# Kernel tuning notes

Hardware: AMD Instinct MI355X
Metric: run time of the kernel (lower is better)

The kernel has to match this reference:

```python
import jax, jax.numpy as jnp
import numpy as np

NH, DH = 16, 64          # n_head, d_head
CH = NH + DH             # 80
RQ, RK, RV = 6, 2, 2
ROPE_BASE = 10000.0


def _rotary(b, cache_len):
    # b: [B, T, R, DH]; rotates the d-factor exactly as the torch Rotary module
    T = b.shape[1]
    inv_freq = (1.0 / ROPE_BASE) ** (jnp.arange(0, DH, 2, dtype=jnp.float32) / DH)
    t = jnp.arange(T, dtype=jnp.float32) + cache_len
    freqs = jnp.outer(t, inv_freq)                      # [T, DH/2]
    cos = freqs[None, :, None, :].astype(b.dtype)
    sin = jnp.sin(freqs)[None, :, None, :].astype(b.dtype)
    cos = jnp.cos(freqs)[None, :, None, :].astype(b.dtype)
    x1, x2 = jnp.split(b, 2, axis=3)
    return jnp.concatenate([x1 * cos + x2 * sin, -x1 * sin + x2 * cos], axis=3)


def setup_inputs() -> dict:
    key = jax.random.key(0)
    k1, k2, k3, k4 = jax.random.split(key, 4)
    B, T, D = 2, 2048, 1024
    x = jax.random.normal(k1, (B, T, D), dtype=jnp.float32)
    # xavier-uniform-like scale for factor projections
    s_q = float(np.sqrt(6.0 / (D + CH)))
    s_o = float(np.sqrt(6.0 / (D + D)))
    W_abq = jax.random.uniform(k2, (RQ * CH, D), minval=-s_q, maxval=s_q, dtype=jnp.float32)
    W_abkv = jax.random.uniform(k3, ((RK + RV) * CH, D), minval=-s_q, maxval=s_q, dtype=jnp.float32)
    W_o = jax.random.uniform(k4, (D, D), minval=-s_o, maxval=s_o, dtype=jnp.float32)
    return {"x": x, "W_abq": W_abq, "W_abkv": W_abkv, "W_o": W_o}


def reference(x, W_abq, W_abkv, W_o):
    B, T, D = x.shape
    # low-rank factor projections
    abq = (x @ W_abq.T).reshape(B, T, RQ, CH)
    a_q, b_q = abq[..., :NH], abq[..., NH:]            # [B,T,RQ,NH], [B,T,RQ,DH]
    abkv = (x @ W_abkv.T).reshape(B, T, RK + RV, CH)
    a_kv = abkv[..., :NH]
    b_kv = _rotary(abkv[..., NH:], cache_len=0)        # RoPE applied to K/V d-factors only
    a_k, b_k = a_kv[:, :, :RK], b_kv[:, :, :RK]
    a_v, b_v = a_kv[:, :, RK:], b_kv[:, :, RK:]
    # tensor-product reconstruction of Q/K/V
    q = jnp.einsum('btrh,btrd->bthd', a_q, b_q) / RQ
    k = jnp.einsum('btrh,btrd->bthd', a_k, b_k) / RK
    v = jnp.einsum('btrh,btrd->bthd', a_v, b_v) / RV
    # causal attention (flex_attention default scale = 1/sqrt(dh))
    scale = 1.0 / jnp.sqrt(jnp.asarray(DH, dtype=q.dtype))
    scores = jnp.einsum('bqhd,bkhd->bhqk', q, k) * scale
    causal = jnp.tril(jnp.ones((T, T), dtype=bool))
    scores = jnp.where(causal[None, None], scores, jnp.finfo(scores.dtype).min)
    attn = jax.nn.softmax(scores, axis=-1)
    y = jnp.einsum('bhqk,bkhd->bqhd', attn, v).reshape(B, T, D)
    return y @ W_o.T
```

## Files before the change

kernel.cpp:

```cpp
#include <hip/hip_runtime.h>
#include <hip/hip_bf16.h>
#include <math.h>

#define NHEADS 16
#define DHEAD  64
#define CHDIM  80
#define RQn    6
#define RKn    2
#define RVn    2
#define BB     2
#define TT     2048
#define DDim   1024
#define NQK    800

using frag16 = __attribute__((ext_vector_type(8))) short;
using f32x4  = __attribute__((ext_vector_type(4))) float;
using f32x16 = __attribute__((ext_vector_type(16))) float;
using uint2v = __attribute__((ext_vector_type(2))) unsigned int;

#define AS1(p) ((const __attribute__((address_space(1))) unsigned int*)(p))
#define AS3(p) ((__attribute__((address_space(3))) unsigned int*)(p))

static __device__ __forceinline__ unsigned short bf16_bits(float f) {
    __hip_bfloat16 h = __float2bfloat16(f);
    return *(unsigned short*)&h;
}
static __device__ __forceinline__ unsigned int pk2(float a, float b) {
    return ((unsigned int)bf16_bits(b) << 16) | (unsigned int)bf16_bits(a);
}
static __device__ __forceinline__ float bfu2f(unsigned short u) {
    return __uint_as_float(((unsigned int)u) << 16);
}
static __device__ __forceinline__ float exp2_hw(float x) {
    return __builtin_amdgcn_exp2f(x);
}

__global__ __launch_bounds__(256) void cvt_all(
    const float* __restrict__ x, const float* __restrict__ wq,
    const float* __restrict__ wk, const float* __restrict__ wo,
    __hip_bfloat16* __restrict__ xb, __hip_bfloat16* __restrict__ wqk,
    __hip_bfloat16* __restrict__ wob)
{
    int bid = blockIdx.x;
    const float* src; __hip_bfloat16* dst; int n4;
    if (bid < 4096)      { src = x;  dst = xb;            n4 = 1048576; }
    else if (bid < 4576) { bid -= 4096; src = wq; dst = wqk;           n4 = 122880; }
    else if (bid < 4896) { bid -= 4576; src = wk; dst = wqk + 491520;  n4 = 81920; }
    else                 { bid -= 4896; src = wo; dst = wob;           n4 = 262144; }
    int i = bid * 256 + threadIdx.x;
    if (i < n4) {
        float4 v = *(const float4*)&src[i * 4];
        ushort4 o;
        o.x = bf16_bits(v.x); o.y = bf16_bits(v.y);
        o.z = bf16_bits(v.z); o.w = bf16_bits(v.w);
        *(ushort4*)&dst[i * 4] = o;
    }
}

template <bool BF16OUT>
__global__ __launch_bounds__(256) void gemm_bf16(
    const __hip_bfloat16* __restrict__ A, const __hip_bfloat16* __restrict__ W,
    void* __restrict__ Cv, int M, int N, int K)
{
    __shared__ __hip_bfloat16 Asl[2][64 * 64];
    __shared__ __hip_bfloat16 Bsl[2][128 * 64];
    const int tid = threadIdx.x;
    const int w = tid >> 6, lane = tid & 63;
    const int l16 = lane & 15, quad = lane >> 4;
    const int bm = blockIdx.y * 64, bn = blockIdx.x * 128;

    int rSA[2], cSA[2];
    #pragma unroll
    for (int j = 0; j < 2; j++) {
        int L = (w * 2 + j) * 64 + lane;
        rSA[j] = L >> 3;
        cSA[j] = (L & 7) ^ (rSA[j] & 7);
    }
    int rSB[4], cSB[4];
    #pragma unroll
    for (int j = 0; j < 4; j++) {
        int L = (w * 4 + j) * 64 + lane;
        int r = L >> 3;
        cSB[j] = (L & 7) ^ (r & 7);
        int rb = bn + r;
        rSB[j] = (rb < N) ? rb : (N - 1);
    }

    f32x4 acc[4][2];
    #pragma unroll
    for (int mt = 0; mt < 4; mt++)
        #pragma unroll
        for (int nt = 0; nt < 2; nt++)
            acc[mt][nt] = (f32x4){0.f, 0.f, 0.f, 0.f};

    const int nK = K >> 6;
    #pragma unroll
    for (int j = 0; j < 2; j++)
        __builtin_amdgcn_global_load_lds(AS1(A + (size_t)(bm + rSA[j]) * K + cSA[j] * 8),
                                         AS3(&Asl[0][(w * 2 + j) * 512]), 16, 0, 0);
    #pragma unroll
    for (int j = 0; j < 4; j++)
        __builtin_amdgcn_global_load_lds(AS1(W + (size_t)rSB[j] * K + cSB[j] * 8),
                                         AS3(&Bsl[0][(w * 4 + j) * 512]), 16, 0, 0);

    for (int kk = 0; kk < nK; kk++) {
        const int cur = kk & 1;
        __syncthreads();
        if (kk + 1 < nK) {
            const int k1 = (kk + 1) * 64;
            #pragma unroll
            for (int j = 0; j < 2; j++)
                __builtin_amdgcn_global_load_lds(AS1(A + (size_t)(bm + rSA[j]) * K + k1 + cSA[j] * 8),
                                                 AS3(&Asl[cur ^ 1][(w * 2 + j) * 512]), 16, 0, 0);
            #pragma unroll
            for (int j = 0; j < 4; j++)
                __builtin_amdgcn_global_load_lds(AS1(W + (size_t)rSB[j] * K + k1 + cSB[j] * 8),
                                                 AS3(&Bsl[cur ^ 1][(w * 4 + j) * 512]), 16, 0, 0);
        }
        #pragma unroll
        for (int ks = 0; ks < 2; ks++) {
            frag16 af[4], bf[2];
            #pragma unroll
            for (int mt = 0; mt < 4; mt++) {
                int r = mt * 16 + l16;
                af[mt] = *(const frag16*)&Asl[cur][r * 64 + (((ks * 4 + quad) ^ (r & 7)) * 8)];
            }
            #pragma unroll
            for (int nt = 0; nt < 2; nt++) {
                int r = w * 32 + nt * 16 + l16;
                bf[nt] = *(const frag16*)&Bsl[cur][r * 64 + (((ks * 4 + quad) ^ (r & 7)) * 8)];
            }
            #pragma unroll
            for (int mt = 0; mt < 4; mt++)
                #pragma unroll
                for (int nt = 0; nt < 2; nt++)
                    acc[mt][nt] = __builtin_amdgcn_mfma_f32_16x16x32_bf16(af[mt], bf[nt], acc[mt][nt], 0, 0, 0);
        }
    }
    #pragma unroll
    for (int mt = 0; mt < 4; mt++) {
        #pragma unroll
        for (int reg = 0; reg < 4; reg++) {
            int row = bm + mt * 16 + quad * 4 + reg;
            #pragma unroll
            for (int nt = 0; nt < 2; nt++) {
                int col = bn + w * 32 + nt * 16 + l16;
                if (col < N) {
                    if constexpr (BF16OUT)
                        ((__hip_bfloat16*)Cv)[(size_t)row * N + col] = __float2bfloat16(acc[mt][nt][reg]);
                    else
                        ((float*)Cv)[(size_t)row * N + col] = acc[mt][nt][reg];
                }
            }
        }
    }
}

__global__ __launch_bounds__(256) void qkv_kernel(
    const __hip_bfloat16* __restrict__ ab,
    __hip_bfloat16* __restrict__ q, __hip_bfloat16* __restrict__ k,
    __hip_bfloat16* __restrict__ vT)
{
    const int tok0 = blockIdx.x * 4;
    const int w = threadIdx.x >> 6;
    const int d = threadIdx.x & 63;
    const int token = tok0 + w;
    const int b = token / TT;
    const int t = token % TT;
    __shared__ float sab[4][NQK];
    __shared__ __align__(8) __hip_bfloat16 vbuf[NHEADS][DHEAD][4];
    const __hip_bfloat16* aq = ab + (size_t)token * NQK;
    #pragma unroll
    for (int i2 = d; i2 < NQK / 2; i2 += 64) {
        unsigned int u = *(const unsigned int*)&aq[i2 * 2];
        sab[w][i2 * 2 + 0] = bfu2f((unsigned short)(u & 0xffff));
        sab[w][i2 * 2 + 1] = bfu2f((unsigned short)(u >> 16));
    }
    const float* sq  = sab[w];
    const float* skv = sab[w] + 480;
    const int i32 = d & 31;
    float inv_freq = exp2_hw(-(float)i32 * (13.287712379549449f / 32.0f));
    float fr = (float)t * inv_freq;
    float c = cosf(fr), s = sinf(fr);
    __syncthreads();
    float rot[4];
    #pragma unroll
    for (int r = 0; r < 4; r++) {
        float x1 = skv[r * CHDIM + NHEADS + i32];
        float x2 = skv[r * CHDIM + NHEADS + 32 + i32];
        rot[r] = (d < 32) ? (x1 * c + x2 * s) : (-x1 * s + x2 * c);
    }
    float bqv[RQn];
    #pragma unroll
    for (int r = 0; r < RQn; r++) bqv[r] = sq[r * CHDIM + NHEADS + d];
    #pragma unroll
    for (int h = 0; h < NHEADS; h++) {
        float accq = 0.0f;
        #pragma unroll
        for (int r = 0; r < RQn; r++)
            accq += sq[r * CHDIM + h] * bqv[r];
        q[((size_t)(b * NHEADS + h) * TT + t) * DHEAD + d] =
            __float2bfloat16(accq * (0.125f / 6.0f) * 1.4426950408889634f);
        float acck = 0.0f, accv = 0.0f;
        #pragma unroll
        for (int r = 0; r < RKn; r++)
            acck += skv[r * CHDIM + h] * rot[r];
        #pragma unroll
        for (int r = 0; r < RVn; r++)
            accv += skv[(RKn + r) * CHDIM + h] * rot[RKn + r];
        k[((size_t)(b * NHEADS + h) * TT + t) * DHEAD + d] = __float2bfloat16(acck * 0.5f);
        vbuf[h][d][w] = __float2bfloat16(accv * 0.5f);
    }
    __syncthreads();
    const int t0 = tok0 % TT;
    const int b0 = tok0 / TT;
    for (int row = threadIdx.x; row < NHEADS * DHEAD; row += 256) {
        int h = row >> 6, dd = row & 63;
        *(uint2*)&vT[((size_t)(b0 * NHEADS + h) * DHEAD + dd) * TT + t0] =
            *(const uint2*)&vbuf[h][dd][0];
    }
}

static __device__ __forceinline__ void build_pfrag(
    const float* s0, const float* s1, frag16 Pf[4])
{
    #pragma unroll
    for (int k2 = 0; k2 < 4; k2++) {
        const float* sF = (k2 >= 2) ? s1 : s0;
        const int bs = 8 * (k2 & 1);
        unsigned int a0 = pk2(sF[bs + 0], sF[bs + 1]);
        unsigned int b0 = pk2(sF[bs + 2], sF[bs + 3]);
        unsigned int a1 = pk2(sF[bs + 4], sF[bs + 5]);
        unsigned int b1 = pk2(sF[bs + 6], sF[bs + 7]);
        uint2v ra = __builtin_amdgcn_permlane32_swap(a0, a1, false, false);
        uint2v rb = __builtin_amdgcn_permlane32_swap(b0, b1, false, false);
        union { frag16 f; unsigned int u[4]; } pf;
        pf.u[0] = ra[0]; pf.u[1] = rb[0]; pf.u[2] = ra[1]; pf.u[3] = rb[1];
        Pf[k2] = pf.f;
    }
}

static __device__ __forceinline__ void attn_tile(
    const __hip_bfloat16* __restrict__ Kc, const __hip_bfloat16* __restrict__ Vc,
    const frag16 qB[4], f32x16& O0, f32x16& O1, float& lpart,
    const int l31, const int hi, const int xi,
    const bool domask, const int kb0, const int qlane)
{
    f32x16 ST0 = {}, ST1 = {};
    __builtin_amdgcn_s_setprio(1);
    #pragma unroll
    for (int kt4 = 0; kt4 < 4; kt4++) {
        int c8 = kt4 * 2 + hi;
        frag16 kf0 = *(const frag16*)&Kc[l31 * 64 + ((c8 ^ xi) * 8)];
        frag16 kf1 = *(const frag16*)&Kc[(32 + l31) * 64 + ((c8 ^ xi) * 8)];
        ST0 = __builtin_amdgcn_mfma_f32_32x32x16_bf16(kf0, qB[kt4], ST0, 0, 0, 0);
        ST1 = __builtin_amdgcn_mfma_f32_32x32x16_bf16(kf1, qB[kt4], ST1, 0, 0, 0);
    }
    __builtin_amdgcn_s_setprio(0);
    float* s0 = (float*)&ST0;
    float* s1 = (float*)&ST1;
    if (domask) {
        int kbq = kb0 + 4 * hi;
        #pragma unroll
        for (int reg = 0; reg < 16; reg++) {
            int rowc = (reg & 3) + 8 * (reg >> 2);
            if (kbq + rowc > qlane)      s0[reg] = -1e30f;
            if (kbq + 32 + rowc > qlane) s1[reg] = -1e30f;
        }
    }
    #pragma unroll
    for (int reg = 0; reg < 16; reg++) {
        float p0 = exp2_hw(s0[reg]);
        float p1 = exp2_hw(s1[reg]);
        s0[reg] = p0; s1[reg] = p1;
        lpart += p0 + p1;
    }
    frag16 Pf[4];
    build_pfrag(s0, s1, Pf);
    __builtin_amdgcn_s_setprio(1);
    #pragma unroll
    for (int k2 = 0; k2 < 4; k2++) {
        int c8 = k2 * 2 + hi;
        frag16 vf0 = *(const frag16*)&Vc[l31 * 64 + ((c8 ^ xi) * 8)];
        frag16 vf1 = *(const frag16*)&Vc[(32 + l31) * 64 + ((c8 ^ xi) * 8)];
        O0 = __builtin_amdgcn_mfma_f32_32x32x16_bf16(vf0, Pf[k2], O0, 0, 0, 0);
        O1 = __builtin_amdgcn_mfma_f32_32x32x16_bf16(vf1, Pf[k2], O1, 0, 0, 0);
    }
    __builtin_amdgcn_s_setprio(0);
}

static __device__ __forceinline__ void attn_tile2(
    const __hip_bfloat16* __restrict__ Kc, const __hip_bfloat16* __restrict__ Vc,
    const frag16 qBlo[4], const frag16 qBhi[4],
    f32x16& Olo0, f32x16& Olo1, float& l_lo,
    f32x16& Ohi0, f32x16& Ohi1, float& l_hi,
    const int l31, const int hi, const int xi,
    const bool domask_lo, const int kb0, const int qlane_lo)
{
    f32x16 SL0 = {}, SL1 = {}, SH0 = {}, SH1 = {};
    __builtin_amdgcn_s_setprio(1);
    #pragma unroll
    for (int kt4 = 0; kt4 < 4; kt4++) {
        int c8 = kt4 * 2 + hi;
        frag16 kf0 = *(const frag16*)&Kc[l31 * 64 + ((c8 ^ xi) * 8)];
        frag16 kf1 = *(const frag16*)&Kc[(32 + l31) * 64 + ((c8 ^ xi) * 8)];
        SL0 = __builtin_amdgcn_mfma_f32_32x32x16_bf16(kf0, qBlo[kt4], SL0, 0, 0, 0);
        SH0 = __builtin_amdgcn_mfma_f32_32x32x16_bf16(kf0, qBhi[kt4], SH0, 0, 0, 0);
        SL1 = __builtin_amdgcn_mfma_f32_32x32x16_bf16(kf1, qBlo[kt4], SL1, 0, 0, 0);
        SH1 = __builtin_amdgcn_mfma_f32_32x32x16_bf16(kf1, qBhi[kt4], SH1, 0, 0, 0);
    }
    __builtin_amdgcn_s_setprio(0);
    float* sl0 = (float*)&SL0; float* sl1 = (float*)&SL1;
    float* sh0 = (float*)&SH0; float* sh1 = (float*)&SH1;
    if (domask_lo) {
        int kbq = kb0 + 4 * hi;
        #pragma unroll
        for (int reg = 0; reg < 16; reg++) {
            int rowc = (reg & 3) + 8 * (reg >> 2);
            if (kbq + rowc > qlane_lo)      sl0[reg] = -1e30f;
            if (kbq + 32 + rowc > qlane_lo) sl1[reg] = -1e30f;
        }
    }
    #pragma unroll
    for (int reg = 0; reg < 16; reg++) {
        float a = exp2_hw(sl0[reg]); float b = exp2_hw(sl1[reg]);
        float c = exp2_hw(sh0[reg]); float d = exp2_hw(sh1[reg]);
        sl0[reg] = a; sl1[reg] = b; sh0[reg] = c; sh1[reg] = d;
        l_lo += a + b; l_hi += c + d;
    }
    frag16 PfL[4], PfH[4];
    build_pfrag(sl0, sl1, PfL);
    build_pfrag(sh0, sh1, PfH);
    __builtin_amdgcn_s_setprio(1);
    #pragma unroll
    for (int k2 = 0; k2 < 4; k2++) {
        int c8 = k2 * 2 + hi;
        frag16 vf0 = *(const frag16*)&Vc[l31 * 64 + ((c8 ^ xi) * 8)];
        frag16 vf1 = *(const frag16*)&Vc[(32 + l31) * 64 + ((c8 ^ xi) * 8)];
        Olo0 = __builtin_amdgcn_mfma_f32_32x32x16_bf16(vf0, PfL[k2], Olo0, 0, 0, 0);
        Ohi0 = __builtin_amdgcn_mfma_f32_32x32x16_bf16(vf0, PfH[k2], Ohi0, 0, 0, 0);
        Olo1 = __builtin_amdgcn_mfma_f32_32x32x16_bf16(vf1, PfL[k2], Olo1, 0, 0, 0);
        Ohi1 = __builtin_amdgcn_mfma_f32_32x32x16_bf16(vf1, PfH[k2], Ohi1, 0, 0, 0);
    }
    __builtin_amdgcn_s_setprio(0);
}

__global__ __launch_bounds__(256, 2) void flash_mfma(
    const __hip_bfloat16* __restrict__ q, const __hip_bfloat16* __restrict__ k,
    const __hip_bfloat16* __restrict__ vT, __hip_bfloat16* __restrict__ y,
    float* __restrict__ Op, float* __restrict__ Lp)
{
    const int Bid = blockIdx.x;
    const int xcd = Bid & 7;
    const int slot0 = Bid >> 3;
    const int bh = xcd * 4 + (slot0 & 3);
    const int idx0 = slot0 >> 2;
    const int qthalf = idx0 & 7;
    const int part = idx0 >> 3;
    const int qt_lo = qthalf, qt_hi = 15 - qthalf;
    const int nlo = 2 * qt_lo + 2;
    const int S = 17 - nlo;
    const int b = bh >> 4, h = bh & 15;
    const int tid = threadIdx.x;
    const int w = tid >> 6;
    const int lane = tid & 63;
    const int l31 = lane & 31;
    const int hi = lane >> 5;
    const int xi = l31 & 7;
    const int paddr = (lane ^ 32) << 2;

    __shared__ __align__(16) __hip_bfloat16 KsF[2][4096];
    __shared__ __align__(16) __hip_bfloat16 VsF[2][4096];

    const size_t base = (size_t)bh * TT * DHEAD;
    const __hip_bfloat16* qb = q + base;
    const __hip_bfloat16* kb = k + base;
    const __hip_bfloat16* vb = vT + base;

    const int ktd_lo = 2 * qt_lo + (w >> 1);
    const int ktd_hi = 2 * qt_hi + (w >> 1);
    const int qlane_lo = qt_lo * 128 + w * 32 + l31;
    const int qlane_hi = qt_hi * 128 + w * 32 + l31;

    const int k0off  = part ? S : 0;
    const int nsteps = part ? 17 : ((nlo > S) ? nlo : S);

    int offK[2], offV[2];
    #pragma unroll
    for (int j = 0; j < 2; j++) {
        int Lc = w * 128 + j * 64 + lane;
        int r = Lc >> 3, c8 = Lc & 7, g8 = c8 ^ (r & 7);
        offK[j] = r * 64 + g8 * 8;
        offV[j] = r * TT + g8 * 8;
    }

    frag16 qB_hi[4], qB_lo[4];
    #pragma unroll
    for (int kt4 = 0; kt4 < 4; kt4++)
        qB_hi[kt4] = *(const frag16*)&qb[(size_t)qlane_hi * DHEAD + kt4 * 16 + hi * 8];
    if (part == 0) {
        #pragma unroll
        for (int kt4 = 0; kt4 < 4; kt4++)
            qB_lo[kt4] = *(const frag16*)&qb[(size_t)qlane_lo * DHEAD + kt4 * 16 + hi * 8];
    }

    f32x16 Olo0 = {}, Olo1 = {}, Ohi0 = {}, Ohi1 = {};
    float l_lo = 0.0f, l_hi = 0.0f;

    #pragma unroll
    for (int j = 0; j < 2; j++) {
        __builtin_amdgcn_global_load_lds(AS1(kb + (size_t)k0off * 4096 + offK[j]),
                                         AS3(&KsF[0][w * 1024 + j * 512]), 16, 0, 0);
        __builtin_amdgcn_global_load_lds(AS1(vb + (size_t)k0off * 64 + offV[j]),
                                         AS3(&VsF[0][w * 1024 + j * 512]), 16, 0, 0);
    }

    for (int kt = 0; kt < nsteps; kt++) {
        const int cur = kt & 1;
        __syncthreads();
        if (kt + 1 < nsteps) {
            const int phys1 = k0off + kt + 1;
            #pragma unroll
            for (int j = 0; j < 2; j++) {
                __builtin_amdgcn_global_load_lds(AS1(kb + (size_t)phys1 * 4096 + offK[j]),
                                                 AS3(&KsF[cur ^ 1][w * 1024 + j * 512]), 16, 0, 0);
                __builtin_amdgcn_global_load_lds(AS1(vb + (size_t)phys1 * 64 + offV[j]),
                                                 AS3(&VsF[cur ^ 1][w * 1024 + j * 512]), 16, 0, 0);
            }
        }
        const __hip_bfloat16* Kc = KsF[cur];
        const __hip_bfloat16* Vc = VsF[cur];
        if (part == 0) {
            const bool do_lo = (kt <= ktd_lo);
            const bool do_hi = (kt < S);
            if (do_lo && do_hi)
                attn_tile2(Kc, Vc, qB_lo, qB_hi, Olo0, Olo1, l_lo, Ohi0, Ohi1, l_hi,
                           l31, hi, xi, kt == ktd_lo, kt * 64, qlane_lo);
            else if (do_lo)
                attn_tile(Kc, Vc, qB_lo, Olo0, Olo1, l_lo, l31, hi, xi,
                          kt == ktd_lo, kt * 64, qlane_lo);
            else if (do_hi)
                attn_tile(Kc, Vc, qB_hi, Ohi0, Ohi1, l_hi, l31, hi, xi,
                          false, 0, qlane_hi);
        } else {
            const int phys = S + kt;
            if (phys <= ktd_hi)
                attn_tile(Kc, Vc, qB_hi, Ohi0, Ohi1, l_hi, l31, hi, xi,
                          phys == ktd_hi, phys * 64, qlane_hi);
        }
    }

    if (part == 0) {
        float lother = __int_as_float(__builtin_amdgcn_ds_bpermute(paddr, __float_as_int(l_lo)));
        float inv = 1.0f / (l_lo + lother);
        float* o0 = (float*)&Olo0;
        float* o1 = (float*)&Olo1;
        __hip_bfloat16* yp = y + ((size_t)(b * TT + qlane_lo)) * DDim + h * DHEAD;
        #pragma unroll
        for (int gg = 0; gg < 4; gg++) {
            int d0 = 8 * gg + 4 * hi;
            uint2 pa, pb;
            pa.x = pk2(o0[4*gg+0] * inv, o0[4*gg+1] * inv);
            pa.y = pk2(o0[4*gg+2] * inv, o0[4*gg+3] * inv);
            pb.x = pk2(o1[4*gg+0] * inv, o1[4*gg+1] * inv);
            pb.y = pk2(o1[4*gg+2] * inv, o1[4*gg+3] * inv);
            *(uint2*)&yp[d0] = pa;
            *(uint2*)&yp[32 + d0] = pb;
        }
    }
    {
        float lother = __int_as_float(__builtin_amdgcn_ds_bpermute(paddr, __float_as_int(l_hi)));
        float ltot = l_hi + lother;
        const int slot = bh * 8 + qthalf;
        const int rloc = w * 32 + l31;
        float* Od = Op + ((size_t)part * 256 + slot) * 8192 + (size_t)rloc * 64;
        float* o0 = (float*)&Ohi0;
        float* o1 = (float*)&Ohi1;
        #pragma unroll
        for (int gg = 0; gg < 4; gg++) {
            int d0 = 8 * gg + 4 * hi;
            *(float4*)&Od[d0]      = (float4){o0[4*gg+0], o0[4*gg+1], o0[4*gg+2], o0[4*gg+3]};
            *(float4*)&Od[32 + d0] = (float4){o1[4*gg+0], o1[4*gg+1], o1[4*gg+2], o1[4*gg+3]};
        }
        if (hi == 0) Lp[part * 32768 + slot * 128 + rloc] = ltot;
    }
}

__global__ __launch_bounds__(256) void combine(
    const float* __restrict__ Op, const float* __restrict__ Lp,
    __hip_bfloat16* __restrict__ y)
{
    int idx = blockIdx.x * 256 + threadIdx.x;
    int cg = (idx & 7) * 8;
    int rowslot = idx >> 3;
    int slot = rowslot >> 7, row = rowslot & 127;
    int bh = slot >> 3, qthalf = slot & 7;
    int b = bh >> 4, h = bh & 15;
    int qrow = (15 - qthalf) * 128 + row;
    float l0 = Lp[slot * 128 + row];
    float l1 = Lp[32768 + slot * 128 + row];
    float inv = 1.0f / (l0 + l1);
    const float* p0 = Op + (size_t)rowslot * 64 + cg;
    const float* p1 = p0 + 2097152;
    __hip_bfloat16* yp = y + ((size_t)(b * TT + qrow)) * DDim + h * DHEAD + cg;
    float4 a0 = *(const float4*)&p0[0];
    float4 a1 = *(const float4*)&p0[4];
    float4 b0 = *(const float4*)&p1[0];
    float4 b1 = *(const float4*)&p1[4];
    uint4 o;
    o.x = pk2((a0.x + b0.x) * inv, (a0.y + b0.y) * inv);
    o.y = pk2((a0.z + b0.z) * inv, (a0.w + b0.w) * inv);
    o.z = pk2((a1.x + b1.x) * inv, (a1.y + b1.y) * inv);
    o.w = pk2((a1.z + b1.z) * inv, (a1.w + b1.w) * inv);
    *(uint4*)&yp[0] = o;
}

extern "C" void kernel_launch(void* const* d_in, const int* in_sizes, int n_in,
                              void* d_out, int out_size, void* d_ws, size_t ws_size,
                              hipStream_t stream) {
    const float* x      = (const float*)d_in[0];
    const float* W_abq  = (const float*)d_in[1];
    const float* W_abkv = (const float*)d_in[2];
    const float* W_o    = (const float*)d_in[3];
    float* out = (float*)d_out;

    char* ws = (char*)d_ws;
    __hip_bfloat16* xb   = (__hip_bfloat16*)ws;  ws += (size_t)4194304 * 2;
    __hip_bfloat16* wqk  = (__hip_bfloat16*)ws;  ws += (size_t)NQK * 1024 * 2;
    __hip_bfloat16* wo_b = (__hip_bfloat16*)ws;  ws += (size_t)1048576 * 2;
    __hip_bfloat16* abqkv = (__hip_bfloat16*)ws; ws += (size_t)4096 * NQK * 2;
    __hip_bfloat16* qb = (__hip_bfloat16*)ws;    ws += (size_t)4194304 * 2;
    __hip_bfloat16* kb = (__hip_bfloat16*)ws;    ws += (size_t)4194304 * 2;
    __hip_bfloat16* vT = (__hip_bfloat16*)ws;    ws += (size_t)4194304 * 2;
    __hip_bfloat16* yb = (__hip_bfloat16*)ws;    ws += (size_t)4194304 * 2;
    float* Op = (float*)ws;                      ws += (size_t)2 * 2097152 * 4;
    float* Lp = (float*)ws;                      ws += (size_t)2 * 32768 * 4;

    cvt_all<<<dim3(5920), dim3(256), 0, stream>>>(x, W_abq, W_abkv, W_o, xb, wqk, wo_b);
    gemm_bf16<true><<<dim3(7, 64), dim3(256), 0, stream>>>(xb, wqk, abqkv, 4096, NQK, 1024);
    qkv_kernel<<<dim3(1024), dim3(256), 0, stream>>>(abqkv, qb, kb, vT);
    flash_mfma<<<dim3(512), dim3(256), 0, stream>>>(qb, kb, vT, yb, Op, Lp);
    combine<<<dim3(1024), dim3(256), 0, stream>>>(Op, Lp, yb);
    gemm_bf16<false><<<dim3(8, 64), dim3(256), 0, stream>>>(yb, wo_b, out, 4096, 1024, 1024);
}
```

Before: 166.2 us.

## Split every query tile's causal KV range in two across blocks, raise occupancy

Replaces the paired lo/hi query-tile scheme, where one block handled two query tiles and wrote the low tile directly, with a uniform scheme. Each of 1024 blocks now handles a single 128-row query tile and one half of its causal KV range. A heavy-first ordering of tiles aims to balance load, and launch bounds are raised to 4 blocks per CU for more occupancy. All partial outputs now go through fp32 Op/Lp buffers and the combine kernel. This doubles the partial-result traffic and combine work, and drops the shared-K/V-tile reuse of the dual-tile MFMA path.

```diff
diff --git a/kernel.cpp b/kernel.cpp
--- a/kernel.cpp
+++ b/kernel.cpp
@@ -289,78 +289,24 @@
     __builtin_amdgcn_s_setprio(0);
 }
 
-static __device__ __forceinline__ void attn_tile2(
-    const __hip_bfloat16* __restrict__ Kc, const __hip_bfloat16* __restrict__ Vc,
-    const frag16 qBlo[4], const frag16 qBhi[4],
-    f32x16& Olo0, f32x16& Olo1, float& l_lo,
-    f32x16& Ohi0, f32x16& Ohi1, float& l_hi,
-    const int l31, const int hi, const int xi,
-    const bool domask_lo, const int kb0, const int qlane_lo)
-{
-    f32x16 SL0 = {}, SL1 = {}, SH0 = {}, SH1 = {};
-    __builtin_amdgcn_s_setprio(1);
-    #pragma unroll
-    for (int kt4 = 0; kt4 < 4; kt4++) {
-        int c8 = kt4 * 2 + hi;
-        frag16 kf0 = *(const frag16*)&Kc[l31 * 64 + ((c8 ^ xi) * 8)];
-        frag16 kf1 = *(const frag16*)&Kc[(32 + l31) * 64 + ((c8 ^ xi) * 8)];
-        SL0 = __builtin_amdgcn_mfma_f32_32x32x16_bf16(kf0, qBlo[kt4], SL0, 0, 0, 0);
-        SH0 = __builtin_amdgcn_mfma_f32_32x32x16_bf16(kf0, qBhi[kt4], SH0, 0, 0, 0);
-        SL1 = __builtin_amdgcn_mfma_f32_32x32x16_bf16(kf1, qBlo[kt4], SL1, 0, 0, 0);
-        SH1 = __builtin_amdgcn_mfma_f32_32x32x16_bf16(kf1, qBhi[kt4], SH1, 0, 0, 0);
-    }
-    __builtin_amdgcn_s_setprio(0);
-    float* sl0 = (float*)&SL0; float* sl1 = (float*)&SL1;
-    float* sh0 = (float*)&SH0; float* sh1 = (float*)&SH1;
-    if (domask_lo) {
-        int kbq = kb0 + 4 * hi;
-        #pragma unroll
-        for (int reg = 0; reg < 16; reg++) {
-            int rowc = (reg & 3) + 8 * (reg >> 2);
-            if (kbq + rowc > qlane_lo)      sl0[reg] = -1e30f;
-            if (kbq + 32 + rowc > qlane_lo) sl1[reg] = -1e30f;
-        }
-    }
-    #pragma unroll
-    for (int reg = 0; reg < 16; reg++) {
-        float a = exp2_hw(sl0[reg]); float b = exp2_hw(sl1[reg]);
-        float c = exp2_hw(sh0[reg]); float d = exp2_hw(sh1[reg]);
-        sl0[reg] = a; sl1[reg] = b; sh0[reg] = c; sh1[reg] = d;
-        l_lo += a + b; l_hi += c + d;
-    }
-    frag16 PfL[4], PfH[4];
-    build_pfrag(sl0, sl1, PfL);
-    build_pfrag(sh0, sh1, PfH);
-    __builtin_amdgcn_s_setprio(1);
-    #pragma unroll
-    for (int k2 = 0; k2 < 4; k2++) {
-        int c8 = k2 * 2 + hi;
-        frag16 vf0 = *(const frag16*)&Vc[l31 * 64 + ((c8 ^ xi) * 8)];
-        frag16 vf1 = *(const frag16*)&Vc[(32 + l31) * 64 + ((c8 ^ xi) * 8)];
-        Olo0 = __builtin_amdgcn_mfma_f32_32x32x16_bf16(vf0, PfL[k2], Olo0, 0, 0, 0);
-        Ohi0 = __builtin_amdgcn_mfma_f32_32x32x16_bf16(vf0, PfH[k2], Ohi0, 0, 0, 0);
-        Olo1 = __builtin_amdgcn_mfma_f32_32x32x16_bf16(vf1, PfL[k2], Olo1, 0, 0, 0);
-        Ohi1 = __builtin_amdgcn_mfma_f32_32x32x16_bf16(vf1, PfH[k2], Ohi1, 0, 0, 0);
-    }
-    __builtin_amdgcn_s_setprio(0);
-}
-
-__global__ __launch_bounds__(256, 2) void flash_mfma(
+__global__ __launch_bounds__(256, 4) void flash_mfma(
     const __hip_bfloat16* __restrict__ q, const __hip_bfloat16* __restrict__ k,
-    const __hip_bfloat16* __restrict__ vT, __hip_bfloat16* __restrict__ y,
+    const __hip_bfloat16* __restrict__ vT,
     float* __restrict__ Op, float* __restrict__ Lp)
 {
     const int Bid = blockIdx.x;
-    const int xcd = Bid & 7;
-    const int slot0 = Bid >> 3;
-    const int bh = xcd * 4 + (slot0 & 3);
-    const int idx0 = slot0 >> 2;
-    const int qthalf = idx0 & 7;
-    const int part = idx0 >> 3;
-    const int qt_lo = qthalf, qt_hi = 15 - qthalf;
-    const int nlo = 2 * qt_lo + 2;
-    const int S = 17 - nlo;
-    const int b = bh >> 4, h = bh & 15;
+    const int m  = Bid & 255;
+    const int g  = Bid >> 8;
+    const int xcd = m & 7;
+    const int bh  = xcd * 4 + ((m >> 3) & 3);
+    const int i8  = m >> 5;
+    const int qtoff = i8 >> 1;
+    const int part  = i8 & 1;
+    const int qt = (g == 0) ? (15 - qtoff) : (g == 1) ? qtoff
+                 : (g == 2) ? (11 - qtoff) : (4 + qtoff);
+    const int nst = qt + 1;
+    const int k0  = part * nst;
+
     const int tid = threadIdx.x;
     const int w = tid >> 6;
     const int lane = tid & 63;
@@ -377,13 +323,8 @@
     const __hip_bfloat16* kb = k + base;
     const __hip_bfloat16* vb = vT + base;
 
-    const int ktd_lo = 2 * qt_lo + (w >> 1);
-    const int ktd_hi = 2 * qt_hi + (w >> 1);
-    const int qlane_lo = qt_lo * 128 + w * 32 + l31;
-    const int qlane_hi = qt_hi * 128 + w * 32 + l31;
-
-    const int k0off  = part ? S : 0;
-    const int nsteps = part ? 17 : ((nlo > S) ? nlo : S);
+    const int ktd = 2 * qt + (w >> 1);
+    const int qlane = qt * 128 + w * 32 + l31;
 
     int offK[2], offV[2];
     #pragma unroll
@@ -394,32 +335,27 @@
         offV[j] = r * TT + g8 * 8;
     }
 
-    frag16 qB_hi[4], qB_lo[4];
+    frag16 qB[4];
     #pragma unroll
     for (int kt4 = 0; kt4 < 4; kt4++)
-        qB_hi[kt4] = *(const frag16*)&qb[(size_t)qlane_hi * DHEAD + kt4 * 16 + hi * 8];
-    if (part == 0) {
-        #pragma unroll
-        for (int kt4 = 0; kt4 < 4; kt4++)
-            qB_lo[kt4] = *(const frag16*)&qb[(size_t)qlane_lo * DHEAD + kt4 * 16 + hi * 8];
-    }
-
-    f32x16 Olo0 = {}, Olo1 = {}, Ohi0 = {}, Ohi1 = {};
-    float l_lo = 0.0f, l_hi = 0.0f;
+        qB[kt4] = *(const frag16*)&qb[(size_t)qlane * DHEAD + kt4 * 16 + hi * 8];
+
+    f32x16 O0 = {}, O1 = {};
+    float l = 0.0f;
 
     #pragma unroll
     for (int j = 0; j < 2; j++) {
-        __builtin_amdgcn_global_load_lds(AS1(kb + (size_t)k0off * 4096 + offK[j]),
+        __builtin_amdgcn_global_load_lds(AS1(kb + (size_t)k0 * 4096 + offK[j]),
                                          AS3(&KsF[0][w * 1024 + j * 512]), 16, 0, 0);
-        __builtin_amdgcn_global_load_lds(AS1(vb + (size_t)k0off * 64 + offV[j]),
+        __builtin_amdgcn_global_load_lds(AS1(vb + (size_t)k0 * 64 + offV[j]),
                                          AS3(&VsF[0][w * 1024 + j * 512]), 16, 0, 0);
     }
 
-    for (int kt = 0; kt < nsteps; kt++) {
+    for (int kt = 0; kt < nst; kt++) {
         const int cur = kt & 1;
         __syncthreads();
-        if (kt + 1 < nsteps) {
-            const int phys1 = k0off + kt + 1;
+        if (kt + 1 < nst) {
+            const int phys1 = k0 + kt + 1;
             #pragma unroll
             for (int j = 0; j < 2; j++) {
                 __builtin_amdgcn_global_load_lds(AS1(kb + (size_t)phys1 * 4096 + offK[j]),
@@ -428,62 +364,26 @@
                                                  AS3(&VsF[cur ^ 1][w * 1024 + j * 512]), 16, 0, 0);
             }
         }
-        const __hip_bfloat16* Kc = KsF[cur];
-        const __hip_bfloat16* Vc = VsF[cur];
-        if (part == 0) {
-            const bool do_lo = (kt <= ktd_lo);
-            const bool do_hi = (kt < S);
-            if (do_lo && do_hi)
-                attn_tile2(Kc, Vc, qB_lo, qB_hi, Olo0, Olo1, l_lo, Ohi0, Ohi1, l_hi,
-                           l31, hi, xi, kt == ktd_lo, kt * 64, qlane_lo);
-            else if (do_lo)
-                attn_tile(Kc, Vc, qB_lo, Olo0, Olo1, l_lo, l31, hi, xi,
-                          kt == ktd_lo, kt * 64, qlane_lo);
-            else if (do_hi)
-                attn_tile(Kc, Vc, qB_hi, Ohi0, Ohi1, l_hi, l31, hi, xi,
-                          false, 0, qlane_hi);
-        } else {
-            const int phys = S + kt;
-            if (phys <= ktd_hi)
-                attn_tile(Kc, Vc, qB_hi, Ohi0, Ohi1, l_hi, l31, hi, xi,
-                          phys == ktd_hi, phys * 64, qlane_hi);
-        }
-    }
-
-    if (part == 0) {
-        float lother = __int_as_float(__builtin_amdgcn_ds_bpermute(paddr, __float_as_int(l_lo)));
-        float inv = 1.0f / (l_lo + lother);
-        float* o0 = (float*)&Olo0;
-        float* o1 = (float*)&Olo1;
-        __hip_bfloat16* yp = y + ((size_t)(b * TT + qlane_lo)) * DDim + h * DHEAD;
-        #pragma unroll
-        for (int gg = 0; gg < 4; gg++) {
-            int d0 = 8 * gg + 4 * hi;
-            uint2 pa, pb;
-            pa.x = pk2(o0[4*gg+0] * inv, o0[4*gg+1] * inv);
-            pa.y = pk2(o0[4*gg+2] * inv, o0[4*gg+3] * inv);
-            pb.x = pk2(o1[4*gg+0] * inv, o1[4*gg+1] * inv);
-            pb.y = pk2(o1[4*gg+2] * inv, o1[4*gg+3] * inv);
-            *(uint2*)&yp[d0] = pa;
-            *(uint2*)&yp[32 + d0] = pb;
-        }
-    }
-    {
-        float lother = __int_as_float(__builtin_amdgcn_ds_bpermute(paddr, __float_as_int(l_hi)));
-        float ltot = l_hi + lother;
-        const int slot = bh * 8 + qthalf;
-        const int rloc = w * 32 + l31;
-        float* Od = Op + ((size_t)part * 256 + slot) * 8192 + (size_t)rloc * 64;
-        float* o0 = (float*)&Ohi0;
-        float* o1 = (float*)&Ohi1;
-        #pragma unroll
-        for (int gg = 0; gg < 4; gg++) {
-            int d0 = 8 * gg + 4 * hi;
-            *(float4*)&Od[d0]      = (float4){o0[4*gg+0], o0[4*gg+1], o0[4*gg+2], o0[4*gg+3]};
-            *(float4*)&Od[32 + d0] = (float4){o1[4*gg+0], o1[4*gg+1], o1[4*gg+2], o1[4*gg+3]};
-        }
-        if (hi == 0) Lp[part * 32768 + slot * 128 + rloc] = ltot;
-    }
+        const int phys = k0 + kt;
+        if (phys <= ktd)
+            attn_tile(KsF[cur], VsF[cur], qB, O0, O1, l, l31, hi, xi,
+                      phys == ktd, phys * 64, qlane);
+    }
+
+    float lother = __int_as_float(__builtin_amdgcn_ds_bpermute(paddr, __float_as_int(l)));
+    float ltot = l + lother;
+    const int slot = bh * 16 + qt;
+    const int rloc = w * 32 + l31;
+    float* Od = Op + ((size_t)part * 512 + slot) * 8192 + (size_t)rloc * 64;
+    float* o0 = (float*)&O0;
+    float* o1 = (float*)&O1;
+    #pragma unroll
+    for (int gg = 0; gg < 4; gg++) {
+        int d0 = 8 * gg + 4 * hi;
+        *(float4*)&Od[d0]      = (float4){o0[4*gg+0], o0[4*gg+1], o0[4*gg+2], o0[4*gg+3]};
+        *(float4*)&Od[32 + d0] = (float4){o1[4*gg+0], o1[4*gg+1], o1[4*gg+2], o1[4*gg+3]};
+    }
+    if (hi == 0) Lp[part * 65536 + slot * 128 + rloc] = ltot;
 }
 
 __global__ __launch_bounds__(256) void combine(
@@ -494,14 +394,14 @@
     int cg = (idx & 7) * 8;
     int rowslot = idx >> 3;
     int slot = rowslot >> 7, row = rowslot & 127;
-    int bh = slot >> 3, qthalf = slot & 7;
+    int bh = slot >> 4, qt = slot & 15;
     int b = bh >> 4, h = bh & 15;
-    int qrow = (15 - qthalf) * 128 + row;
+    int qrow = qt * 128 + row;
     float l0 = Lp[slot * 128 + row];
-    float l1 = Lp[32768 + slot * 128 + row];
+    float l1 = Lp[65536 + slot * 128 + row];
     float inv = 1.0f / (l0 + l1);
     const float* p0 = Op + (size_t)rowslot * 64 + cg;
-    const float* p1 = p0 + 2097152;
+    const float* p1 = p0 + 4194304;
     __hip_bfloat16* yp = y + ((size_t)(b * TT + qrow)) * DDim + h * DHEAD + cg;
     float4 a0 = *(const float4*)&p0[0];
     float4 a1 = *(const float4*)&p0[4];
@@ -533,13 +433,13 @@
     __hip_bfloat16* kb = (__hip_bfloat16*)ws;    ws += (size_t)4194304 * 2;
     __hip_bfloat16* vT = (__hip_bfloat16*)ws;    ws += (size_t)4194304 * 2;
     __hip_bfloat16* yb = (__hip_bfloat16*)ws;    ws += (size_t)4194304 * 2;
-    float* Op = (float*)ws;                      ws += (size_t)2 * 2097152 * 4;
-    float* Lp = (float*)ws;                      ws += (size_t)2 * 32768 * 4;
+    float* Op = (float*)ws;                      ws += (size_t)2 * 4194304 * 4;
+    float* Lp = (float*)ws;                      ws += (size_t)2 * 65536 * 4;
 
     cvt_all<<<dim3(5920), dim3(256), 0, stream>>>(x, W_abq, W_abkv, W_o, xb, wqk, wo_b);
     gemm_bf16<true><<<dim3(7, 64), dim3(256), 0, stream>>>(xb, wqk, abqkv, 4096, NQK, 1024);
     qkv_kernel<<<dim3(1024), dim3(256), 0, stream>>>(abqkv, qb, kb, vT);
-    flash_mfma<<<dim3(512), dim3(256), 0, stream>>>(qb, kb, vT, yb, Op, Lp);
-    combine<<<dim3(1024), dim3(256), 0, stream>>>(Op, Lp, yb);
+    flash_mfma<<<dim3(1024), dim3(256), 0, stream>>>(qb, kb, vT, Op, Lp);
+    combine<<<dim3(2048), dim3(256), 0, stream>>>(Op, Lp, yb);
     gemm_bf16<false><<<dim3(8, 64), dim3(256), 0, stream>>>(yb, wo_b, out, 4096, 1024, 1024);
 }
```

New measurement: 166.5 us. Within noise of the previous version (+0.2%).
